# Kernel optimization log

Hardware: AMD Instinct MI355X
Metric: run time of the kernel (lower is better)

Reference implementation:

```python
import jax, jax.numpy as jnp
import numpy as np
from jax.ops import segment_sum

N_NODES = 50000


def gcn_conv(x, src, dst, W, b, n_nodes):
    # PyG GCNConv with default add_self_loops=True, normalize=True.
    # deg includes self-loops (weight 1 each).
    deg = segment_sum(jnp.ones_like(dst, dtype=x.dtype), dst, num_segments=n_nodes) + 1.0
    dinv = jax.lax.rsqrt(deg)  # [N]
    h = x @ W                  # [N, out]
    # messages over real edges: norm[src]*norm[dst]*h[src]
    msg = h[src] * (dinv[src] * dinv[dst])[:, None]   # [E, out]
    agg = segment_sum(msg, dst, num_segments=n_nodes)  # [N, out]
    # self-loop contribution: dinv[i]^2 * h[i]
    agg = agg + h * (dinv * dinv)[:, None]
    return agg + b


def setup_inputs() -> dict:
    key = jax.random.key(0)
    k1, k2, k3, k4 = jax.random.split(key, 4)
    N, E, d_in, d_hid, d_out = N_NODES, 800000, 128, 128, 64
    x = jax.random.normal(k1, (N, d_in), dtype=jnp.float32)
    edge_index = jax.random.randint(k2, (2, E), 0, N, dtype=jnp.int64)
    W1 = jax.random.normal(k3, (d_in, d_hid), dtype=jnp.float32) / np.sqrt(d_in)
    b1 = jnp.zeros((d_hid,), dtype=jnp.float32)
    W2 = jax.random.normal(k4, (d_hid, d_out), dtype=jnp.float32) / np.sqrt(d_hid)
    b2 = jnp.zeros((d_out,), dtype=jnp.float32)
    return {"x": x, "edge_index": edge_index, "W1": W1, "b1": b1, "W2": W2, "b2": b2}


def reference(x, edge_index, W1, b1, W2, b2):
    src, dst = edge_index[0], edge_index[1]
    h = gcn_conv(x, src, dst, W1, b1, N_NODES)
    h = jax.nn.relu(h)
    out = gcn_conv(h, src, dst, W2, b2, N_NODES)
    return out
```

## Files before the change

### kernel.cpp

```cpp
#include <hip/hip_runtime.h>
#include <hip/hip_bf16.h>


#define ELL_CAP 64
#define NPART 8

typedef __attribute__((ext_vector_type(8))) short short8;
typedef __attribute__((ext_vector_type(4))) float f32x4;

static __device__ __forceinline__ unsigned short f2bf(float f) {
    unsigned int u = __float_as_uint(f);
    u = (u + 0x7fff + ((u >> 16) & 1)) >> 16;
    return (unsigned short)u;
}
static __device__ __forceinline__ float2 bfunpack(unsigned int u) {
    return make_float2(__uint_as_float(u << 16),
                       __uint_as_float(u & 0xffff0000u));
}


__global__ void zero_cnt(int* __restrict__ cnt, int n) {
    int i = blockIdx.x * blockDim.x + threadIdx.x;
    if (i < n) cnt[i] = 0;
}

__global__ __launch_bounds__(256) void build_ell_part(
    const int* __restrict__ src, const int* __restrict__ dst,
    int* __restrict__ cnt, int* __restrict__ ell, int E, int partSize)
{
    const int part   = blockIdx.x & (NPART - 1);
    const int chunk  = blockIdx.x >> 3;
    const int nchunk = gridDim.x >> 3;
    const int lo = part * partSize, hi = lo + partSize;
    const int per = (E + nchunk - 1) / nchunk;
    const int e1 = min((chunk + 1) * per, E);
    for (int e = chunk * per + threadIdx.x; e < e1; e += 256) {
        int d = dst[e];
        if (d >= lo && d < hi) {
            int pos = atomicAdd(&cnt[d], 1);
            if (pos < ELL_CAP) ell[(size_t)d * ELL_CAP + pos] = src[e];
        }
    }
}

__global__ void convert_weights(const float* __restrict__ W1, const float* __restrict__ W2,
                                short* __restrict__ w1t, short* __restrict__ w2t)
{
    int i = blockIdx.x * blockDim.x + threadIdx.x;
    if (i < 128 * 128) {
        int k = i >> 7, nn = i & 127;
        w1t[nn * 128 + k] = (short)f2bf(W1[i]);
    } else if (i < 128 * 128 + 128 * 64) {
        int j = i - 128 * 128;
        int k = j >> 6, nn = j & 63;
        w2t[nn * 128 + k] = (short)f2bf(W2[j]);
    }
}


template<int NC, bool AF32>
__global__ __launch_bounds__(256) void gemm_mfma(
    const void* __restrict__ Av, const short* __restrict__ Bt,
    const int* __restrict__ cnt, unsigned short* __restrict__ Cb, int n)
{
    __shared__ short Bs[NC][136];
    const int tid = threadIdx.x;

    #pragma unroll
    for (int i = 0; i < NC / 16; ++i) {
        int idx = tid + i * 256;
        int nrow = idx >> 4;
        int kcol = (idx & 15) * 8;
        *(short8*)&Bs[nrow][kcol] = *(const short8*)(Bt + nrow * 128 + kcol);
    }
    __syncthreads();

    const int wave = tid >> 6, lane = tid & 63;
    const int row0 = blockIdx.x * 64 + wave * 16;
    if (row0 >= n) return;
    const int quad = lane >> 4, l16 = lane & 15;

    short8 af[4];
    if (AF32) {
        const float* arow = (const float*)Av + (size_t)(row0 + l16) * 128 + quad * 8;
        #pragma unroll
        for (int kk = 0; kk < 4; ++kk) {
            float4 u = *(const float4*)(arow + kk * 32);
            float4 v = *(const float4*)(arow + kk * 32 + 4);
            short8 f;
            f[0] = (short)f2bf(u.x); f[1] = (short)f2bf(u.y);
            f[2] = (short)f2bf(u.z); f[3] = (short)f2bf(u.w);
            f[4] = (short)f2bf(v.x); f[5] = (short)f2bf(v.y);
            f[6] = (short)f2bf(v.z); f[7] = (short)f2bf(v.w);
            af[kk] = f;
        }
    } else {
        const short* arow = (const short*)Av + (size_t)(row0 + l16) * 128 + quad * 8;
        #pragma unroll
        for (int kk = 0; kk < 4; ++kk)
            af[kk] = *(const short8*)(arow + kk * 32);
    }

    float dv[4];
    #pragma unroll
    for (int r = 0; r < 4; ++r)
        dv[r] = rsqrtf((float)cnt[row0 + quad * 4 + r] + 1.0f);

    #pragma unroll
    for (int t = 0; t < NC / 16; ++t) {
        f32x4 acc = {0.f, 0.f, 0.f, 0.f};
        #pragma unroll
        for (int kk = 0; kk < 4; ++kk) {
            short8 bfr = *(const short8*)&Bs[t * 16 + l16][kk * 32 + quad * 8];
            acc = __builtin_amdgcn_mfma_f32_16x16x32_bf16(af[kk], bfr, acc, 0, 0, 0);
        }
        #pragma unroll
        for (int r = 0; r < 4; ++r) {
            int gr = row0 + quad * 4 + r;
            Cb[(size_t)gr * NC + t * 16 + l16] = f2bf(acc[r] * dv[r]);
        }
    }
}


__global__ __launch_bounds__(256) void aggregate_l1(
    const unsigned int* __restrict__ hp, const int* __restrict__ ell,
    const int* __restrict__ cnt, const float* __restrict__ bias,
    unsigned int* __restrict__ z1b, int n)
{
    int node = blockIdx.x * 4 + (threadIdx.x >> 6);
    if (node >= n) return;
    int lane = threadIdx.x & 63;
    int deg = cnt[node];
    float d = rsqrtf((float)deg + 1.0f);
    if (deg > ELL_CAP) deg = ELL_CAP;
    const int* __restrict__ row = ell + (size_t)node * ELL_CAP;

    float2 acc = bfunpack(hp[(size_t)node * 64 + lane]);
    int e = 0;
    for (; e + 4 <= deg; e += 4) {
        int s0 = row[e], s1 = row[e + 1], s2 = row[e + 2], s3 = row[e + 3];
        float2 v0 = bfunpack(hp[(size_t)s0 * 64 + lane]);
        float2 v1 = bfunpack(hp[(size_t)s1 * 64 + lane]);
        float2 v2 = bfunpack(hp[(size_t)s2 * 64 + lane]);
        float2 v3 = bfunpack(hp[(size_t)s3 * 64 + lane]);
        acc.x += (v0.x + v1.x) + (v2.x + v3.x);
        acc.y += (v0.y + v1.y) + (v2.y + v3.y);
    }
    for (; e < deg; ++e) {
        float2 v = bfunpack(hp[(size_t)row[e] * 64 + lane]);
        acc.x += v.x; acc.y += v.y;
    }
    float ox = fmaxf(fmaf(acc.x, d, bias[lane * 2]), 0.f);
    float oy = fmaxf(fmaf(acc.y, d, bias[lane * 2 + 1]), 0.f);
    z1b[(size_t)node * 64 + lane] =
        (unsigned int)f2bf(ox) | ((unsigned int)f2bf(oy) << 16);
}


__global__ __launch_bounds__(256) void aggregate_l2(
    const unsigned int* __restrict__ hp, const int* __restrict__ ell,
    const int* __restrict__ cnt, const float* __restrict__ bias,
    float* __restrict__ out, int n)
{
    int lane = threadIdx.x & 63;
    int half = lane >> 5, l32 = lane & 31;
    int node = blockIdx.x * 8 + (threadIdx.x >> 6) * 2 + half;
    if (node >= n) return;
    int deg = cnt[node];
    float d = rsqrtf((float)deg + 1.0f);
    if (deg > ELL_CAP) deg = ELL_CAP;
    const int* __restrict__ row = ell + (size_t)node * ELL_CAP;

    float2 acc = bfunpack(hp[(size_t)node * 32 + l32]);
    int e = 0;
    for (; e + 4 <= deg; e += 4) {
        int s0 = row[e], s1 = row[e + 1], s2 = row[e + 2], s3 = row[e + 3];
        float2 v0 = bfunpack(hp[(size_t)s0 * 32 + l32]);
        float2 v1 = bfunpack(hp[(size_t)s1 * 32 + l32]);
        float2 v2 = bfunpack(hp[(size_t)s2 * 32 + l32]);
        float2 v3 = bfunpack(hp[(size_t)s3 * 32 + l32]);
        acc.x += (v0.x + v1.x) + (v2.x + v3.x);
        acc.y += (v0.y + v1.y) + (v2.y + v3.y);
    }
    for (; e < deg; ++e) {
        float2 v = bfunpack(hp[(size_t)row[e] * 32 + l32]);
        acc.x += v.x; acc.y += v.y;
    }
    float2 o;
    o.x = fmaf(acc.x, d, bias[l32 * 2]);
    o.y = fmaf(acc.y, d, bias[l32 * 2 + 1]);
    ((float2*)out)[(size_t)node * 32 + l32] = o;
}


extern "C" void kernel_launch(void* const* d_in, const int* in_sizes, int n_in,
                              void* d_out, int out_size, void* d_ws, size_t ws_size,
                              hipStream_t stream)
{
    const float* x  = (const float*)d_in[0];
    const int*   ei = (const int*)d_in[1];
    const float* W1 = (const float*)d_in[2];
    const float* b1 = (const float*)d_in[3];
    const float* W2 = (const float*)d_in[4];
    const float* b2 = (const float*)d_in[5];
    float* out = (float*)d_out;

    const int N = in_sizes[0] / 128;
    const int E = in_sizes[1] / 2;
    const int* src = ei;
    const int* dst = ei + E;
    const int partSize = (N + NPART - 1) / NPART;

    char* ws = (char*)d_ws;
    size_t off = 0;
    auto alloc = [&](size_t bytes) -> void* {
        void* p = ws + off;
        off += (bytes + 255) & ~(size_t)255;
        return p;
    };
    int*            cnt  = (int*)           alloc((size_t)N * 4);
    int*            ell  = (int*)           alloc((size_t)N * ELL_CAP * 4);
    short*          w1t  = (short*)         alloc((size_t)128 * 128 * 2);
    short*          w2t  = (short*)         alloc((size_t)64 * 128 * 2);
    unsigned short* h1b  = (unsigned short*)alloc((size_t)N * 128 * 2);
    unsigned int*   z1b  = (unsigned int*)  alloc((size_t)N * 64 * 4);
    unsigned short* h2b  = (unsigned short*)alloc((size_t)N * 64 * 2);

    convert_weights<<<(128 * 192 + 255) / 256, 256, 0, stream>>>(W1, W2, w1t, w2t);
    zero_cnt<<<(N + 255) / 256, 256, 0, stream>>>(cnt, N);
    build_ell_part<<<128 * NPART, 256, 0, stream>>>(src, dst, cnt, ell, E, partSize);

    gemm_mfma<128, true><<<(N + 63) / 64, 256, 0, stream>>>(x, w1t, cnt, h1b, N);
    aggregate_l1<<<(N + 3) / 4, 256, 0, stream>>>((const unsigned int*)h1b, ell, cnt, b1, z1b, N);

    gemm_mfma<64, false><<<(N + 63) / 64, 256, 0, stream>>>(z1b, w2t, cnt, h2b, N);
    aggregate_l2<<<(N + 7) / 8, 256, 0, stream>>>((const unsigned int*)h2b, ell, cnt, b2, out, N);
}
```

Measured before the change: 197.0 us.

## Store ELL indices as 16-bit, vectorize edge scan, fuse init kernels

ELL neighbor indices are stored as unsigned short instead of int, halving index memory traffic in both aggregation kernels, which now load four indices with one 8-byte read. The ELL build reads src/dst as int4 and runs more chunk blocks, and weight conversion is merged with count zeroing into one kernel to drop a launch. The 16-bit indices assume fewer than 65536 nodes, and the narrow scattered stores during the build may be less efficient.

```diff
diff --git a/kernel.cpp b/kernel.cpp
--- a/kernel.cpp
+++ b/kernel.cpp
@@ -19,32 +19,9 @@
 }
 
 
-__global__ void zero_cnt(int* __restrict__ cnt, int n) {
-    int i = blockIdx.x * blockDim.x + threadIdx.x;
-    if (i < n) cnt[i] = 0;
-}
-
-__global__ __launch_bounds__(256) void build_ell_part(
-    const int* __restrict__ src, const int* __restrict__ dst,
-    int* __restrict__ cnt, int* __restrict__ ell, int E, int partSize)
-{
-    const int part   = blockIdx.x & (NPART - 1);
-    const int chunk  = blockIdx.x >> 3;
-    const int nchunk = gridDim.x >> 3;
-    const int lo = part * partSize, hi = lo + partSize;
-    const int per = (E + nchunk - 1) / nchunk;
-    const int e1 = min((chunk + 1) * per, E);
-    for (int e = chunk * per + threadIdx.x; e < e1; e += 256) {
-        int d = dst[e];
-        if (d >= lo && d < hi) {
-            int pos = atomicAdd(&cnt[d], 1);
-            if (pos < ELL_CAP) ell[(size_t)d * ELL_CAP + pos] = src[e];
-        }
-    }
-}
-
-__global__ void convert_weights(const float* __restrict__ W1, const float* __restrict__ W2,
-                                short* __restrict__ w1t, short* __restrict__ w2t)
+__global__ void init_misc(const float* __restrict__ W1, const float* __restrict__ W2,
+                          short* __restrict__ w1t, short* __restrict__ w2t,
+                          int* __restrict__ cnt, int n)
 {
     int i = blockIdx.x * blockDim.x + threadIdx.x;
     if (i < 128 * 128) {
@@ -54,6 +31,54 @@
         int j = i - 128 * 128;
         int k = j >> 6, nn = j & 63;
         w2t[nn * 128 + k] = (short)f2bf(W2[j]);
+    }
+    if (i < n) cnt[i] = 0;
+}
+
+
+__global__ __launch_bounds__(256) void build_ell_part(
+    const int* __restrict__ src, const int* __restrict__ dst,
+    int* __restrict__ cnt, unsigned short* __restrict__ ell, int E, int partSize)
+{
+    const int part   = blockIdx.x & (NPART - 1);
+    const int chunk  = blockIdx.x >> 3;
+    const int nchunk = gridDim.x >> 3;
+    const int lo = part * partSize, hi = lo + partSize;
+
+    const int  E4  = E >> 2;
+    const int  per = (E4 + nchunk - 1) / nchunk;
+    const int  i1  = min((chunk + 1) * per, E4);
+    const int4* __restrict__ d4p = (const int4*)dst;
+    const int4* __restrict__ s4p = (const int4*)src;
+
+    for (int i = chunk * per + threadIdx.x; i < i1; i += 256) {
+        int4 d4 = d4p[i];
+        int4 s4 = s4p[i];
+        if (d4.x >= lo && d4.x < hi) {
+            int p = atomicAdd(&cnt[d4.x], 1);
+            if (p < ELL_CAP) ell[(size_t)d4.x * ELL_CAP + p] = (unsigned short)s4.x;
+        }
+        if (d4.y >= lo && d4.y < hi) {
+            int p = atomicAdd(&cnt[d4.y], 1);
+            if (p < ELL_CAP) ell[(size_t)d4.y * ELL_CAP + p] = (unsigned short)s4.y;
+        }
+        if (d4.z >= lo && d4.z < hi) {
+            int p = atomicAdd(&cnt[d4.z], 1);
+            if (p < ELL_CAP) ell[(size_t)d4.z * ELL_CAP + p] = (unsigned short)s4.z;
+        }
+        if (d4.w >= lo && d4.w < hi) {
+            int p = atomicAdd(&cnt[d4.w], 1);
+            if (p < ELL_CAP) ell[(size_t)d4.w * ELL_CAP + p] = (unsigned short)s4.w;
+        }
+    }
+    if (chunk == 0) {
+        for (int e = (E & ~3) + threadIdx.x; e < E; e += 256) {
+            int d = dst[e];
+            if (d >= lo && d < hi) {
+                int p = atomicAdd(&cnt[d], 1);
+                if (p < ELL_CAP) ell[(size_t)d * ELL_CAP + p] = (unsigned short)src[e];
+            }
+        }
     }
 }
 
@@ -124,7 +149,7 @@
 
 
 __global__ __launch_bounds__(256) void aggregate_l1(
-    const unsigned int* __restrict__ hp, const int* __restrict__ ell,
+    const unsigned int* __restrict__ hp, const unsigned short* __restrict__ ell,
     const int* __restrict__ cnt, const float* __restrict__ bias,
     unsigned int* __restrict__ z1b, int n)
 {
@@ -134,12 +159,14 @@
     int deg = cnt[node];
     float d = rsqrtf((float)deg + 1.0f);
     if (deg > ELL_CAP) deg = ELL_CAP;
-    const int* __restrict__ row = ell + (size_t)node * ELL_CAP;
+    const unsigned short* __restrict__ row = ell + (size_t)node * ELL_CAP;
 
     float2 acc = bfunpack(hp[(size_t)node * 64 + lane]);
     int e = 0;
     for (; e + 4 <= deg; e += 4) {
-        int s0 = row[e], s1 = row[e + 1], s2 = row[e + 2], s3 = row[e + 3];
+        uint2 w = *(const uint2*)&row[e];
+        int s0 = w.x & 0xffff, s1 = w.x >> 16;
+        int s2 = w.y & 0xffff, s3 = w.y >> 16;
         float2 v0 = bfunpack(hp[(size_t)s0 * 64 + lane]);
         float2 v1 = bfunpack(hp[(size_t)s1 * 64 + lane]);
         float2 v2 = bfunpack(hp[(size_t)s2 * 64 + lane]);
@@ -159,7 +186,7 @@
 
 
 __global__ __launch_bounds__(256) void aggregate_l2(
-    const unsigned int* __restrict__ hp, const int* __restrict__ ell,
+    const unsigned int* __restrict__ hp, const unsigned short* __restrict__ ell,
     const int* __restrict__ cnt, const float* __restrict__ bias,
     float* __restrict__ out, int n)
 {
@@ -170,12 +197,14 @@
     int deg = cnt[node];
     float d = rsqrtf((float)deg + 1.0f);
     if (deg > ELL_CAP) deg = ELL_CAP;
-    const int* __restrict__ row = ell + (size_t)node * ELL_CAP;
+    const unsigned short* __restrict__ row = ell + (size_t)node * ELL_CAP;
 
     float2 acc = bfunpack(hp[(size_t)node * 32 + l32]);
     int e = 0;
     for (; e + 4 <= deg; e += 4) {
-        int s0 = row[e], s1 = row[e + 1], s2 = row[e + 2], s3 = row[e + 3];
+        uint2 w = *(const uint2*)&row[e];
+        int s0 = w.x & 0xffff, s1 = w.x >> 16;
+        int s2 = w.y & 0xffff, s3 = w.y >> 16;
         float2 v0 = bfunpack(hp[(size_t)s0 * 32 + l32]);
         float2 v1 = bfunpack(hp[(size_t)s1 * 32 + l32]);
         float2 v2 = bfunpack(hp[(size_t)s2 * 32 + l32]);
@@ -220,16 +249,15 @@
         return p;
     };
     int*            cnt  = (int*)           alloc((size_t)N * 4);
-    int*            ell  = (int*)           alloc((size_t)N * ELL_CAP * 4);
+    unsigned short* ell  = (unsigned short*)alloc((size_t)N * ELL_CAP * 2);
     short*          w1t  = (short*)         alloc((size_t)128 * 128 * 2);
     short*          w2t  = (short*)         alloc((size_t)64 * 128 * 2);
     unsigned short* h1b  = (unsigned short*)alloc((size_t)N * 128 * 2);
     unsigned int*   z1b  = (unsigned int*)  alloc((size_t)N * 64 * 4);
     unsigned short* h2b  = (unsigned short*)alloc((size_t)N * 64 * 2);
 
-    convert_weights<<<(128 * 192 + 255) / 256, 256, 0, stream>>>(W1, W2, w1t, w2t);
-    zero_cnt<<<(N + 255) / 256, 256, 0, stream>>>(cnt, N);
-    build_ell_part<<<128 * NPART, 256, 0, stream>>>(src, dst, cnt, ell, E, partSize);
+    init_misc<<<(N + 255) / 256, 256, 0, stream>>>(W1, W2, w1t, w2t, cnt, N);
+    build_ell_part<<<256 * NPART, 256, 0, stream>>>(src, dst, cnt, ell, E, partSize);
 
     gemm_mfma<128, true><<<(N + 63) / 64, 256, 0, stream>>>(x, w1t, cnt, h1b, N);
     aggregate_l1<<<(N + 3) / 4, 256, 0, stream>>>((const unsigned int*)h1b, ell, cnt, b1, z1b, N);
```

Measured after the change: 197.4 us. Within noise of the previous version (+0.2%).
